# Optimization experiments

Hardware: AMD Instinct MI355X
Metric: run time of the kernel (lower is better)

Reference implementation:

```python
import jax, jax.numpy as jnp
import numpy as np
import math

B, M, N = 1, 128, 256
LIG_C = 256      # rep_1d num_c
ATTN_C = 32      # attention_num_c
HEADS = 8        # num_heads
EPS = 1e-5


def setup_inputs() -> dict:
    key = jax.random.key(0)
    ks = jax.random.split(key, 8)
    s = 1.0 / math.sqrt(LIG_C)
    return {
        "lig_profile": jax.random.normal(ks[0], (B, M, N, LIG_C), dtype=jnp.float32),
        "ln_scale": jnp.ones((LIG_C,), dtype=jnp.float32),
        "ln_bias": jnp.zeros((LIG_C,), dtype=jnp.float32),
        "wq": jax.random.normal(ks[1], (LIG_C, ATTN_C * HEADS), dtype=jnp.float32) * s,
        "wk": jax.random.normal(ks[2], (LIG_C, ATTN_C * HEADS), dtype=jnp.float32) * s,
        "wv": jax.random.normal(ks[3], (LIG_C, ATTN_C * HEADS), dtype=jnp.float32) * s,
        "wf": jax.random.normal(ks[4], (ATTN_C * HEADS, LIG_C), dtype=jnp.float32) * s,
        "bf": jnp.zeros((LIG_C,), dtype=jnp.float32),
    }


def reference(lig_profile, ln_scale, ln_bias, wq, wk, wv, wf, bf):
    # LayerNorm over channel dim
    mu = jnp.mean(lig_profile, axis=-1, keepdims=True)
    var = jnp.mean(jnp.square(lig_profile - mu), axis=-1, keepdims=True)
    x = (lig_profile - mu) * jax.lax.rsqrt(var + EPS) * ln_scale + ln_bias

    # QKV projections; view splits last dim as (attn_c, heads) -> channel-major layout
    shape5 = x.shape[:-1] + (ATTN_C, HEADS)
    q = (x @ wq).reshape(shape5)  # [b,m,n,c,h]
    k = (x @ wk).reshape(shape5)
    v = (x @ wv).reshape(shape5)

    factor = 1.0 / math.sqrt(ATTN_C)
    aff = jnp.einsum('bmich,bmjch->bmijh', q, k) * factor  # [b,m,i,j,h]
    weights = jax.nn.softmax(aff, axis=-2)                  # softmax over j (keys)
    out = jnp.einsum('bmrch,bmirh->bmich', v, weights)      # [b,m,i,c,h]
    out = out.reshape(out.shape[:-2] + (ATTN_C * HEADS,))
    return out @ wf + bf
```

## Files before the change

### kernel.cpp

```cpp
#include <hip/hip_runtime.h>

typedef _Float16 f16;
typedef _Float16 f16x8 __attribute__((ext_vector_type(8)));
typedef _Float16 f16x4 __attribute__((ext_vector_type(4)));
typedef _Float16 f16x2 __attribute__((ext_vector_type(2)));
typedef float f32x4 __attribute__((ext_vector_type(4)));
typedef float f32x16 __attribute__((ext_vector_type(16)));

#define MDIM 128
#define NDIM 256
#define CDIM 256
#define ROWS (MDIM*NDIM)
#define L2E 1.4426950408889634f

__device__ inline int pk2(float a, float b) {
  union { f16x2 h; int i; } u;
  u.h[0] = (f16)a; u.h[1] = (f16)b;
  return u.i;
}

__global__ __launch_bounds__(256) void k_prep(
    const float* __restrict__ wq, const float* __restrict__ wk,
    const float* __restrict__ wv, const float* __restrict__ wf,
    f16* __restrict__ bq, f16* __restrict__ bk, f16* __restrict__ bv,
    f16* __restrict__ bw)
{
  __shared__ f16 ld[64][264];
  int which = blockIdx.x >> 2, kb = blockIdx.x & 3;
  int t = threadIdx.x;
  int k0 = kb * 64;
  if (which < 3) {
    const float* W = which == 0 ? wq : which == 1 ? wk : wv;
    f16* dst       = which == 0 ? bq : which == 1 ? bk : bv;
    float sc = which == 0 ? 0.17677669529663689f : 1.0f;
    for (int r = 0; r < 64; ++r)
      ld[r][t] = (f16)(W[(size_t)(k0 + r) * 256 + t] * sc);
    __syncthreads();
    int j = (t & 31) * 8 + (t >> 5);
#pragma unroll
    for (int rr = 0; rr < 8; ++rr) {
      f16x8 o;
#pragma unroll
      for (int i = 0; i < 8; ++i) o[i] = ld[rr * 8 + i][j];
      *(f16x8*)(dst + (size_t)t * 256 + k0 + rr * 8) = o;
    }
  } else {
    for (int r = 0; r < 64; ++r) {
      int ke = k0 + r;
      int jr = (ke & 31) * 8 + (ke >> 5);
      ld[r][t] = (f16)wf[(size_t)jr * 256 + t];
    }
    __syncthreads();
#pragma unroll
    for (int rr = 0; rr < 8; ++rr) {
      f16x8 o;
#pragma unroll
      for (int i = 0; i < 8; ++i) o[i] = ld[rr * 8 + i][t];
      *(f16x8*)(bw + (size_t)t * 256 + k0 + rr * 8) = o;
    }
  }
}

__global__ __launch_bounds__(512) void k_lnqkv(const float* __restrict__ x,
    const float* __restrict__ g, const float* __restrict__ bb,
    const f16* __restrict__ bq, const f16* __restrict__ bk, const f16* __restrict__ bv,
    f16* __restrict__ qo, f16* __restrict__ ko, f16* __restrict__ vT)
{
  __shared__ f16 As[64][264];
  __shared__ f16 vtmp[8][16][72];
  int bm = blockIdx.x;
  int t = threadIdx.x, lane = t & 63, w = t >> 6;
  int l15 = lane & 15, l4 = lane >> 4;
  const float4 gv  = *(const float4*)(g + lane * 4);
  const float4 bv4 = *(const float4*)(bb + lane * 4);
#pragma unroll
  for (int rr = 0; rr < 8; ++rr) {
    int r = w * 8 + rr;
    const float4 xv = *(const float4*)(x + (size_t)(bm * 64 + r) * 256 + lane * 4);
    float s  = xv.x + xv.y + xv.z + xv.w;
    float s2 = xv.x*xv.x + xv.y*xv.y + xv.z*xv.z + xv.w*xv.w;
#pragma unroll
    for (int mm = 1; mm < 64; mm <<= 1) {
      s  += __shfl_xor(s,  mm, 64);
      s2 += __shfl_xor(s2, mm, 64);
    }
    float mu  = s * (1.0f / 256.0f);
    float var = s2 * (1.0f / 256.0f) - mu * mu;
    float rs  = rsqrtf(var + 1e-5f);
    f16x4 ov;
    ov[0] = (f16)((xv.x - mu) * rs * gv.x + bv4.x);
    ov[1] = (f16)((xv.y - mu) * rs * gv.y + bv4.y);
    ov[2] = (f16)((xv.z - mu) * rs * gv.z + bv4.z);
    ov[3] = (f16)((xv.w - mu) * rs * gv.w + bv4.w);
    *(f16x4*)&As[r][lane * 4] = ov;
  }
  __syncthreads();
  for (int it = 0; it < 2; ++it) {
    int gc0 = it * 384 + w * 48;
    f32x4 acc[4][3] = {};
#pragma unroll
    for (int kt = 0; kt < 8; ++kt) {
      f16x8 af[4];
#pragma unroll
      for (int mi = 0; mi < 4; ++mi)
        af[mi] = *(const f16x8*)&As[mi * 16 + l15][kt * 32 + l4 * 8];
#pragma unroll
      for (int ni = 0; ni < 3; ++ni) {
        int gc = gc0 + ni * 16;
        const f16* B = gc < 256 ? bq : gc < 512 ? bk : bv;
        f16x8 bf = *(const f16x8*)(B + (size_t)((gc & 255) + l15) * 256 + kt * 32 + l4 * 8);
#pragma unroll
        for (int mi = 0; mi < 4; ++mi)
          acc[mi][ni] = __builtin_amdgcn_mfma_f32_16x16x32_f16(af[mi], bf, acc[mi][ni], 0, 0, 0);
      }
    }
#pragma unroll
    for (int ni = 0; ni < 3; ++ni) {
      int gc = gc0 + ni * 16;
      if (gc < 512) {
        f16* dst = gc < 256 ? qo : ko;
        int col = (gc & 255) + l15;
#pragma unroll
        for (int mi = 0; mi < 4; ++mi)
#pragma unroll
          for (int r = 0; r < 4; ++r)
            dst[(size_t)(bm * 64 + mi * 16 + l4 * 4 + r) * 256 + col] = (f16)acc[mi][ni][r];
      } else {
#pragma unroll
        for (int mi = 0; mi < 4; ++mi)
#pragma unroll
          for (int r = 0; r < 4; ++r)
            vtmp[w][l15][mi * 16 + l4 * 4 + r] = (f16)acc[mi][ni][r];
        int ch = lane >> 2, nq = (lane & 3) * 16;
        f16x8 v0 = *(const f16x8*)&vtmp[w][ch][nq];
        f16x8 v1 = *(const f16x8*)&vtmp[w][ch][nq + 8];
        size_t gdst = ((size_t)(bm >> 2) * 256 + (gc & 255) + ch) * 256 + (bm & 3) * 64 + nq;
        *(f16x8*)(vT + gdst)     = v0;
        *(f16x8*)(vT + gdst + 8) = v1;
      }
    }
  }
}

__global__ __launch_bounds__(512, 4) void k_attn(const f16* __restrict__ q,
    const f16* __restrict__ k, const f16* __restrict__ vT, f16* __restrict__ o)
{
  __shared__ f16 ks[256][40];
  __shared__ f16 vt[32][264];
  int bx = blockIdx.x;
  int m = bx >> 3, h = bx & 7;
  int t = threadIdx.x, lane = t & 63, w = t >> 6;
  int i32 = lane & 31, hi = lane >> 5;
  size_t rowbase = (size_t)m * 256;
#pragma unroll
  for (int p = 0; p < 2; ++p) {
    int n = p * 128 + (t >> 2);
    int c0 = (t & 3) * 8;
    *(f16x8*)&ks[n][c0] = *(const f16x8*)(k + (rowbase + n) * 256 + h * 32 + c0);
  }
#pragma unroll
  for (int p = 0; p < 2; ++p) {
    int idx = p * 512 + t;
    int c = idx >> 5, nb = (idx & 31) * 8;
    *(f16x8*)&vt[c][nb] = *(const f16x8*)(vT + ((size_t)m * 256 + h * 32 + c) * 256 + nb);
  }
  __syncthreads();
  int qi0 = w * 32;
  const f16* qp = q + (rowbase + qi0 + i32) * 256 + h * 32 + hi * 8;
  f16x8 qf0 = *(const f16x8*)(qp);
  f16x8 qf1 = *(const f16x8*)(qp + 16);
  f32x16 O = {};
  float m_run = -1e30f, l_run = 0.f;
#pragma unroll 2
  for (int kb = 0; kb < 8; ++kb) {
    f16x8 kf0 = *(const f16x8*)&ks[kb * 32 + i32][hi * 8];
    f16x8 kf1 = *(const f16x8*)&ks[kb * 32 + i32][16 + hi * 8];
    f32x16 s = {};
    __builtin_amdgcn_s_setprio(1);
    s = __builtin_amdgcn_mfma_f32_32x32x16_f16(kf0, qf0, s, 0, 0, 0);
    s = __builtin_amdgcn_mfma_f32_32x32x16_f16(kf1, qf1, s, 0, 0, 0);
    __builtin_amdgcn_s_setprio(0);
#pragma unroll
    for (int r = 0; r < 16; ++r) s[r] *= L2E;
    float pmax = s[0];
#pragma unroll
    for (int r = 1; r < 16; ++r) pmax = fmaxf(pmax, s[r]);
    pmax = fmaxf(pmax, __shfl_xor(pmax, 32, 64));
    if (!__all(pmax - m_run <= 8.f)) {
      float m_new = fmaxf(m_run, pmax);
      float f = __builtin_amdgcn_exp2f(m_run - m_new);
      l_run *= f;
#pragma unroll
      for (int r = 0; r < 16; ++r)
        O[r] *= __shfl(f, (r & 3) + 8 * (r >> 2) + 4 * hi, 64);
      m_run = m_new;
    }
    float lsum = 0.f;
#pragma unroll
    for (int r = 0; r < 16; ++r) {
      float e = __builtin_amdgcn_exp2f(s[r] - m_run);
      s[r] = e;
      lsum += e;
    }
    lsum += __shfl_xor(lsum, 32, 64);
    l_run += lsum;
    int W0[4], W1[4];
#pragma unroll
    for (int qq = 0; qq < 4; ++qq) {
      W0[qq] = pk2(s[4 * qq],     s[4 * qq + 1]);
      W1[qq] = pk2(s[4 * qq + 2], s[4 * qq + 3]);
    }
#pragma unroll
    for (int ks2 = 0; ks2 < 2; ++ks2) {
      int X0 = W0[2 * ks2], Y0 = W0[2 * ks2 + 1];
      int X1 = W1[2 * ks2], Y1 = W1[2 * ks2 + 1];
      int a0 = __shfl(X0, i32, 64),      b0 = __shfl(Y0, i32, 64);
      int a1 = __shfl(X1, i32, 64),      b1 = __shfl(Y1, i32, 64);
      int a2 = __shfl(X0, i32 + 32, 64), b2 = __shfl(Y0, i32 + 32, 64);
      int a3 = __shfl(X1, i32 + 32, 64), b3 = __shfl(Y1, i32 + 32, 64);
      union { unsigned int ww[4]; f16x8 v; } pa;
      pa.ww[0] = hi ? (unsigned)b0 : (unsigned)a0;
      pa.ww[1] = hi ? (unsigned)b1 : (unsigned)a1;
      pa.ww[2] = hi ? (unsigned)b2 : (unsigned)a2;
      pa.ww[3] = hi ? (unsigned)b3 : (unsigned)a3;
      f16x8 vb = *(const f16x8*)&vt[i32][kb * 32 + ks2 * 16 + hi * 8];
      __builtin_amdgcn_s_setprio(1);
      O = __builtin_amdgcn_mfma_f32_32x32x16_f16(pa.v, vb, O, 0, 0, 0);
      __builtin_amdgcn_s_setprio(0);
    }
  }
  float inv = 1.f / l_run;
#pragma unroll
  for (int r = 0; r < 16; ++r) {
    int i = (r & 3) + 8 * (r >> 2) + 4 * hi;
    float fr = __shfl(inv, i, 64);
    o[(rowbase + (size_t)(qi0 + i)) * 256 + h * 32 + i32] = (f16)(O[r] * fr);
  }
}

__global__ __launch_bounds__(512) void k_out(const f16* __restrict__ a,
    const f16* __restrict__ bw, const float* __restrict__ bias,
    float* __restrict__ out)
{
  __shared__ f16 As[64][264];
  int bm = blockIdx.x;
  int t = threadIdx.x, lane = t & 63, w = t >> 6;
  int l15 = lane & 15, l4 = lane >> 4;
#pragma unroll
  for (int p = 0; p < 4; ++p) {
    int idx = p * 512 + t;
    int r = idx >> 5, c0 = (idx & 31) * 8;
    *(f16x8*)&As[r][c0] = *(const f16x8*)(a + (size_t)(bm * 64 + r) * 256 + c0);
  }
  __syncthreads();
  int gc0 = w * 32;
  f32x4 acc[4][2] = {};
#pragma unroll
  for (int kt = 0; kt < 8; ++kt) {
    f16x8 af[4];
#pragma unroll
    for (int mi = 0; mi < 4; ++mi)
      af[mi] = *(const f16x8*)&As[mi * 16 + l15][kt * 32 + l4 * 8];
#pragma unroll
    for (int ni = 0; ni < 2; ++ni) {
      f16x8 bf = *(const f16x8*)(bw + (size_t)(gc0 + ni * 16 + l15) * 256 + kt * 32 + l4 * 8);
#pragma unroll
      for (int mi = 0; mi < 4; ++mi)
        acc[mi][ni] = __builtin_amdgcn_mfma_f32_16x16x32_f16(af[mi], bf, acc[mi][ni], 0, 0, 0);
    }
  }
  float b0 = bias[gc0 + l15], b1 = bias[gc0 + 16 + l15];
#pragma unroll
  for (int mi = 0; mi < 4; ++mi)
#pragma unroll
    for (int r = 0; r < 4; ++r) {
      int row = bm * 64 + mi * 16 + l4 * 4 + r;
      out[(size_t)row * 256 + gc0 + l15]      = acc[mi][0][r] + b0;
      out[(size_t)row * 256 + gc0 + 16 + l15] = acc[mi][1][r] + b1;
    }
}

extern "C" void kernel_launch(void* const* d_in, const int* in_sizes, int n_in,
                              void* d_out, int out_size, void* d_ws, size_t ws_size,
                              hipStream_t stream)
{
  const float* x  = (const float*)d_in[0];
  const float* g  = (const float*)d_in[1];
  const float* b  = (const float*)d_in[2];
  const float* wq = (const float*)d_in[3];
  const float* wk = (const float*)d_in[4];
  const float* wv = (const float*)d_in[5];
  const float* wf = (const float*)d_in[6];
  const float* bf = (const float*)d_in[7];
  float* out = (float*)d_out;

  char* ws = (char*)d_ws;
  f16* ah  = (f16*)(ws);
  f16* qh  = (f16*)(ws + (size_t)16 * 1024 * 1024);
  f16* kh  = (f16*)(ws + (size_t)32 * 1024 * 1024);
  f16* vTh = (f16*)(ws + (size_t)48 * 1024 * 1024);
  char* wbase = ws + (size_t)64 * 1024 * 1024;
  f16* bq = (f16*)(wbase);
  f16* bk = (f16*)(wbase + 128 * 1024);
  f16* bv = (f16*)(wbase + 256 * 1024);
  f16* bw = (f16*)(wbase + 384 * 1024);

  k_prep <<<16,   256, 0, stream>>>(wq, wk, wv, wf, bq, bk, bv, bw);
  k_lnqkv<<<512,  512, 0, stream>>>(x, g, b, bq, bk, bv, qh, kh, vTh);
  k_attn <<<1024, 512, 0, stream>>>(qh, kh, vTh, ah);
  k_out  <<<512,  512, 0, stream>>>(ah, bw, bf, out);
}
```

Before: 95.14 us.

## Split LayerNorm from QKV GEMM and retile projection GEMMs over 2D grids

LayerNorm moves out of the fused LN+QKV kernel into its own kernel that writes an fp16 normalized buffer. The QKV GEMM is retiled on a 2D grid where each wave computes a 64x64 tile with operands loaded straight from global memory instead of LDS. The output projection is likewise retiled into smaller 2D-grid blocks without LDS staging, with launch bounds raised for occupancy. This adds a round trip through an extra fp16 activation buffer and an extra launch, in exchange for more parallelism and fewer LDS barriers.

```diff
diff --git a/kernel.cpp b/kernel.cpp
--- a/kernel.cpp
+++ b/kernel.cpp
@@ -61,83 +61,89 @@
   }
 }
 
-__global__ __launch_bounds__(512) void k_lnqkv(const float* __restrict__ x,
-    const float* __restrict__ g, const float* __restrict__ bb,
+__global__ __launch_bounds__(256) void k_ln(const float* __restrict__ x,
+                                            const float* __restrict__ g,
+                                            const float* __restrict__ b,
+                                            f16* __restrict__ y)
+{
+  int row  = blockIdx.x * 4 + (threadIdx.x >> 6);
+  int lane = threadIdx.x & 63;
+  const float4 xv = *(const float4*)(x + (size_t)row * CDIM + lane * 4);
+  float s  = xv.x + xv.y + xv.z + xv.w;
+  float s2 = xv.x*xv.x + xv.y*xv.y + xv.z*xv.z + xv.w*xv.w;
+#pragma unroll
+  for (int m = 1; m < 64; m <<= 1) {
+    s  += __shfl_xor(s,  m, 64);
+    s2 += __shfl_xor(s2, m, 64);
+  }
+  float mu  = s * (1.0f / CDIM);
+  float var = s2 * (1.0f / CDIM) - mu * mu;
+  float rs  = rsqrtf(var + 1e-5f);
+  const float4 gv = *(const float4*)(g + lane * 4);
+  const float4 bv = *(const float4*)(b + lane * 4);
+  f16x4 o;
+  o[0] = (f16)((xv.x - mu) * rs * gv.x + bv.x);
+  o[1] = (f16)((xv.y - mu) * rs * gv.y + bv.y);
+  o[2] = (f16)((xv.z - mu) * rs * gv.z + bv.z);
+  o[3] = (f16)((xv.w - mu) * rs * gv.w + bv.w);
+  *(f16x4*)(y + (size_t)row * CDIM + lane * 4) = o;
+}
+
+__global__ __launch_bounds__(256, 4) void k_qkv(const f16* __restrict__ xh,
     const f16* __restrict__ bq, const f16* __restrict__ bk, const f16* __restrict__ bv,
     f16* __restrict__ qo, f16* __restrict__ ko, f16* __restrict__ vT)
 {
-  __shared__ f16 As[64][264];
-  __shared__ f16 vtmp[8][16][72];
+  __shared__ f16 vtmp[4][16][72];
   int bm = blockIdx.x;
+  int ct = blockIdx.y;
   int t = threadIdx.x, lane = t & 63, w = t >> 6;
+  int wr = w >> 1, wc = w & 1;
   int l15 = lane & 15, l4 = lane >> 4;
-  const float4 gv  = *(const float4*)(g + lane * 4);
-  const float4 bv4 = *(const float4*)(bb + lane * 4);
-#pragma unroll
-  for (int rr = 0; rr < 8; ++rr) {
-    int r = w * 8 + rr;
-    const float4 xv = *(const float4*)(x + (size_t)(bm * 64 + r) * 256 + lane * 4);
-    float s  = xv.x + xv.y + xv.z + xv.w;
-    float s2 = xv.x*xv.x + xv.y*xv.y + xv.z*xv.z + xv.w*xv.w;
-#pragma unroll
-    for (int mm = 1; mm < 64; mm <<= 1) {
-      s  += __shfl_xor(s,  mm, 64);
-      s2 += __shfl_xor(s2, mm, 64);
-    }
-    float mu  = s * (1.0f / 256.0f);
-    float var = s2 * (1.0f / 256.0f) - mu * mu;
-    float rs  = rsqrtf(var + 1e-5f);
-    f16x4 ov;
-    ov[0] = (f16)((xv.x - mu) * rs * gv.x + bv4.x);
-    ov[1] = (f16)((xv.y - mu) * rs * gv.y + bv4.y);
-    ov[2] = (f16)((xv.z - mu) * rs * gv.z + bv4.z);
-    ov[3] = (f16)((xv.w - mu) * rs * gv.w + bv4.w);
-    *(f16x4*)&As[r][lane * 4] = ov;
-  }
-  __syncthreads();
-  for (int it = 0; it < 2; ++it) {
-    int gc0 = it * 384 + w * 48;
-    f32x4 acc[4][3] = {};
-#pragma unroll
-    for (int kt = 0; kt < 8; ++kt) {
-      f16x8 af[4];
+  int r0  = bm * 128 + wr * 64;
+  int gc0 = ct * 128 + wc * 64;
+  int sec = gc0 >> 8;
+  const f16* B = sec == 0 ? bq : sec == 1 ? bk : bv;
+  int c0 = gc0 & 255;
+  f32x4 acc[4][4] = {};
+#pragma unroll
+  for (int kt = 0; kt < 8; ++kt) {
+    f16x8 af[4], bf[4];
+#pragma unroll
+    for (int mi = 0; mi < 4; ++mi)
+      af[mi] = *(const f16x8*)(xh + (size_t)(r0 + mi * 16 + l15) * 256 + kt * 32 + l4 * 8);
+#pragma unroll
+    for (int ni = 0; ni < 4; ++ni)
+      bf[ni] = *(const f16x8*)(B + (size_t)(c0 + ni * 16 + l15) * 256 + kt * 32 + l4 * 8);
+#pragma unroll
+    for (int mi = 0; mi < 4; ++mi)
+#pragma unroll
+      for (int ni = 0; ni < 4; ++ni)
+        acc[mi][ni] = __builtin_amdgcn_mfma_f32_16x16x32_f16(af[mi], bf[ni], acc[mi][ni], 0, 0, 0);
+  }
+  if (sec < 2) {
+    f16* dst = sec == 0 ? qo : ko;
+#pragma unroll
+    for (int mi = 0; mi < 4; ++mi)
+#pragma unroll
+      for (int ni = 0; ni < 4; ++ni)
+#pragma unroll
+        for (int r = 0; r < 4; ++r)
+          dst[(size_t)(r0 + mi * 16 + l4 * 4 + r) * 256 + c0 + ni * 16 + l15] = (f16)acc[mi][ni][r];
+  } else {
+    int m = bm >> 1, n0 = (bm & 1) * 128 + wr * 64;
+    int ch = lane >> 2, nq = (lane & 3) * 16;
+#pragma unroll
+    for (int ni = 0; ni < 4; ++ni) {
 #pragma unroll
       for (int mi = 0; mi < 4; ++mi)
-        af[mi] = *(const f16x8*)&As[mi * 16 + l15][kt * 32 + l4 * 8];
-#pragma unroll
-      for (int ni = 0; ni < 3; ++ni) {
-        int gc = gc0 + ni * 16;
-        const f16* B = gc < 256 ? bq : gc < 512 ? bk : bv;
-        f16x8 bf = *(const f16x8*)(B + (size_t)((gc & 255) + l15) * 256 + kt * 32 + l4 * 8);
-#pragma unroll
-        for (int mi = 0; mi < 4; ++mi)
-          acc[mi][ni] = __builtin_amdgcn_mfma_f32_16x16x32_f16(af[mi], bf, acc[mi][ni], 0, 0, 0);
-      }
-    }
-#pragma unroll
-    for (int ni = 0; ni < 3; ++ni) {
-      int gc = gc0 + ni * 16;
-      if (gc < 512) {
-        f16* dst = gc < 256 ? qo : ko;
-        int col = (gc & 255) + l15;
-#pragma unroll
-        for (int mi = 0; mi < 4; ++mi)
-#pragma unroll
-          for (int r = 0; r < 4; ++r)
-            dst[(size_t)(bm * 64 + mi * 16 + l4 * 4 + r) * 256 + col] = (f16)acc[mi][ni][r];
-      } else {
-#pragma unroll
-        for (int mi = 0; mi < 4; ++mi)
-#pragma unroll
-          for (int r = 0; r < 4; ++r)
-            vtmp[w][l15][mi * 16 + l4 * 4 + r] = (f16)acc[mi][ni][r];
-        int ch = lane >> 2, nq = (lane & 3) * 16;
-        f16x8 v0 = *(const f16x8*)&vtmp[w][ch][nq];
-        f16x8 v1 = *(const f16x8*)&vtmp[w][ch][nq + 8];
-        size_t gdst = ((size_t)(bm >> 2) * 256 + (gc & 255) + ch) * 256 + (bm & 3) * 64 + nq;
-        *(f16x8*)(vT + gdst)     = v0;
-        *(f16x8*)(vT + gdst + 8) = v1;
-      }
+#pragma unroll
+        for (int r = 0; r < 4; ++r)
+          vtmp[w][l15][mi * 16 + l4 * 4 + r] = (f16)acc[mi][ni][r];
+      f16x8 v0 = *(const f16x8*)&vtmp[w][ch][nq];
+      f16x8 v1 = *(const f16x8*)&vtmp[w][ch][nq + 8];
+      size_t gdst = ((size_t)m * 256 + c0 + ni * 16 + ch) * 256 + n0 + nq;
+      *(f16x8*)(vT + gdst)     = v0;
+      *(f16x8*)(vT + gdst + 8) = v1;
     }
   }
 }
@@ -238,45 +244,41 @@
   }
 }
 
-__global__ __launch_bounds__(512) void k_out(const f16* __restrict__ a,
+__global__ __launch_bounds__(256, 4) void k_out(const f16* __restrict__ a,
     const f16* __restrict__ bw, const float* __restrict__ bias,
     float* __restrict__ out)
 {
-  __shared__ f16 As[64][264];
   int bm = blockIdx.x;
+  int ct = blockIdx.y;
   int t = threadIdx.x, lane = t & 63, w = t >> 6;
+  int wr = w >> 1, wc = w & 1;
   int l15 = lane & 15, l4 = lane >> 4;
-#pragma unroll
-  for (int p = 0; p < 4; ++p) {
-    int idx = p * 512 + t;
-    int r = idx >> 5, c0 = (idx & 31) * 8;
-    *(f16x8*)&As[r][c0] = *(const f16x8*)(a + (size_t)(bm * 64 + r) * 256 + c0);
-  }
-  __syncthreads();
-  int gc0 = w * 32;
-  f32x4 acc[4][2] = {};
+  int r0 = bm * 64 + wr * 32;
+  int c0 = ct * 64 + wc * 32;
+  f32x4 acc[2][2] = {};
 #pragma unroll
   for (int kt = 0; kt < 8; ++kt) {
-    f16x8 af[4];
-#pragma unroll
-    for (int mi = 0; mi < 4; ++mi)
-      af[mi] = *(const f16x8*)&As[mi * 16 + l15][kt * 32 + l4 * 8];
-#pragma unroll
-    for (int ni = 0; ni < 2; ++ni) {
-      f16x8 bf = *(const f16x8*)(bw + (size_t)(gc0 + ni * 16 + l15) * 256 + kt * 32 + l4 * 8);
-#pragma unroll
-      for (int mi = 0; mi < 4; ++mi)
-        acc[mi][ni] = __builtin_amdgcn_mfma_f32_16x16x32_f16(af[mi], bf, acc[mi][ni], 0, 0, 0);
-    }
-  }
-  float b0 = bias[gc0 + l15], b1 = bias[gc0 + 16 + l15];
-#pragma unroll
-  for (int mi = 0; mi < 4; ++mi)
+    f16x8 af[2], bf[2];
+#pragma unroll
+    for (int mi = 0; mi < 2; ++mi)
+      af[mi] = *(const f16x8*)(a + (size_t)(r0 + mi * 16 + l15) * 256 + kt * 32 + l4 * 8);
+#pragma unroll
+    for (int ni = 0; ni < 2; ++ni)
+      bf[ni] = *(const f16x8*)(bw + (size_t)(c0 + ni * 16 + l15) * 256 + kt * 32 + l4 * 8);
+#pragma unroll
+    for (int mi = 0; mi < 2; ++mi)
+#pragma unroll
+      for (int ni = 0; ni < 2; ++ni)
+        acc[mi][ni] = __builtin_amdgcn_mfma_f32_16x16x32_f16(af[mi], bf[ni], acc[mi][ni], 0, 0, 0);
+  }
+  float b0 = bias[c0 + l15], b1 = bias[c0 + 16 + l15];
+#pragma unroll
+  for (int mi = 0; mi < 2; ++mi)
 #pragma unroll
     for (int r = 0; r < 4; ++r) {
-      int row = bm * 64 + mi * 16 + l4 * 4 + r;
-      out[(size_t)row * 256 + gc0 + l15]      = acc[mi][0][r] + b0;
-      out[(size_t)row * 256 + gc0 + 16 + l15] = acc[mi][1][r] + b1;
+      int row = r0 + mi * 16 + l4 * 4 + r;
+      out[(size_t)row * 256 + c0 + l15]      = acc[mi][0][r] + b0;
+      out[(size_t)row * 256 + c0 + 16 + l15] = acc[mi][1][r] + b1;
     }
 }
 
@@ -295,7 +297,7 @@
   float* out = (float*)d_out;
 
   char* ws = (char*)d_ws;
-  f16* ah  = (f16*)(ws);
+  f16* xh  = (f16*)(ws);
   f16* qh  = (f16*)(ws + (size_t)16 * 1024 * 1024);
   f16* kh  = (f16*)(ws + (size_t)32 * 1024 * 1024);
   f16* vTh = (f16*)(ws + (size_t)48 * 1024 * 1024);
@@ -304,9 +306,11 @@
   f16* bk = (f16*)(wbase + 128 * 1024);
   f16* bv = (f16*)(wbase + 256 * 1024);
   f16* bw = (f16*)(wbase + 384 * 1024);
-
-  k_prep <<<16,   256, 0, stream>>>(wq, wk, wv, wf, bq, bk, bv, bw);
-  k_lnqkv<<<512,  512, 0, stream>>>(x, g, b, bq, bk, bv, qh, kh, vTh);
-  k_attn <<<1024, 512, 0, stream>>>(qh, kh, vTh, ah);
-  k_out  <<<512,  512, 0, stream>>>(ah, bw, bf, out);
-}
+  f16* ah = (f16*)(ws + (size_t)80 * 1024 * 1024);
+
+  k_prep<<<16,                256, 0, stream>>>(wq, wk, wv, wf, bq, bk, bv, bw);
+  k_ln  <<<ROWS / 4,          256, 0, stream>>>(x, g, b, xh);
+  k_qkv <<<dim3(256, 6),      256, 0, stream>>>(xh, bq, bk, bv, qh, kh, vTh);
+  k_attn<<<1024,              512, 0, stream>>>(qh, kh, vTh, ah);
+  k_out <<<dim3(512, 4),      256, 0, stream>>>(ah, bw, bf, out);
+}
```

Result: slower. 135.6 us (+42.6%).
